# Kernel optimization log

Measured on AMD Instinct MI355X. Metric: run time of the kernel, lower is better.

The kernel has to match this reference:

```python
import jax, jax.numpy as jnp
import numpy as np

# ---- configuration matching init_kwargs ----
CTX_C = 96        # context_v_features
M_FREQS = 8       # m_encode_num_freqs
OUT_C = 45        # out_features
NDIM = 3
SIGMA = 5.0       # sigma_encode_scale
EPS = 1e-7        # TARGET_COORD_EPSILON
CX = CY = CZ = 32
QX = QY = QZ = 48
B = 1
CTX_VOX = 2.0
Q_VOX = 1.25
N_COORD = 4 * NDIM + NDIM * 2 * M_FREQS   # 60
INTERNAL = CTX_C + N_COORD                # 156


def _lin_init(k, fi, fo):
    s = 1.0 / np.sqrt(fi)
    kw, kb = jax.random.split(k)
    return (jax.random.uniform(kw, (fi, fo), jnp.float32, -s, s),
            jax.random.uniform(kb, (fo,), jnp.float32, -s, s))


def setup_inputs() -> dict:
    key = jax.random.key(0)
    ks = jax.random.split(key, 12)
    context_v = jax.random.normal(ks[0], (B, CTX_C, CX, CY, CZ), jnp.float32)
    ax = jnp.arange(CX, dtype=jnp.float32) * CTX_VOX
    gx, gy, gz = jnp.meshgrid(ax, ax, ax, indexing='ij')
    context_spatial_extent = jnp.broadcast_to(
        jnp.stack([gx, gy, gz], 0)[None], (B, 3, CX, CY, CZ)).astype(jnp.float32)
    # queries in the interior so nearest-idx + 1 stays in bounds
    query_coord = jax.random.uniform(ks[1], (B, 3, QX, QY, QZ), jnp.float32,
                                     CTX_VOX, (CX - 2) * CTX_VOX)
    query_vox_size = jnp.full((B, 3), Q_VOX, jnp.float32)
    inp = dict(context_v=context_v, context_spatial_extent=context_spatial_extent,
               query_vox_size=query_vox_size, query_coord=query_coord)
    ki = 2
    for b in range(2):
        inp[f'blk{b}_w0'], inp[f'blk{b}_b0'] = _lin_init(ks[ki], INTERNAL, CTX_C); ki += 1
        inp[f'blk{b}_w1'], inp[f'blk{b}_b1'] = _lin_init(ks[ki], CTX_C, CTX_C); ki += 1
        inp[f'blk{b}_w2'], inp[f'blk{b}_b2'] = _lin_init(ks[ki], CTX_C, CTX_C); ki += 1
    inp['post_w'], inp['post_b'] = _lin_init(ks[ki], CTX_C, OUT_C)
    return inp


def _flat(t):
    # 'b c x y z -> (b x y z) c'
    return jnp.moveaxis(t, 1, -1).reshape(-1, t.shape[1])


def _unflat(t, b, x, y, z):
    # '(b x y z) c -> b c x y z'
    return jnp.moveaxis(t.reshape(b, x, y, z, -1), -1, 1)


def _fourier(c):
    # c: (N, 3) normalized coords; geometric frequency ladder scaled by sigma
    freqs = SIGMA ** (jnp.arange(M_FREQS, dtype=c.dtype) / M_FREQS)   # (m,)
    ang = (2.0 * jnp.pi) * c[:, :, None] * freqs                      # (N,3,m)
    return jnp.concatenate([jnp.sin(ang), jnp.cos(ang)], axis=-1).reshape(c.shape[0], -1)


def _skip_block(x, coord, w0, b0, w1, b1, w2, b2):
    # SkipMLPBlock: concat(context, coord) -> 3 dense SiLU layers -> residual add
    h = jnp.concatenate([x, coord], axis=-1)
    h = jax.nn.silu(h @ w0 + b0)
    h = jax.nn.silu(h @ w1 + b1)
    h = jax.nn.silu(h @ w2 + b2)
    return x + h, coord


def _sub_grid_forward(ctx_val, ctx_coord, q_coord, ctx_vox, q_vox, p):
    # ctx_val: (B,C,X,Y,Z); coords: (B,3,X,Y,Z); ctx_vox/q_vox: (B,3,1,1,1)
    b, _, x, y, z = q_coord.shape
    rel = jnp.maximum(ctx_coord - q_coord, -ctx_vox / 2 + EPS)
    rel_norm = (rel - jnp.min(rel, axis=(2, 3, 4), keepdims=True)) / (1.5 * ctx_vox)
    enc = _fourier(_flat(rel_norm))                                   # (N, 6m)
    qv = jnp.broadcast_to(q_vox, rel_norm.shape)
    coord_feats = jnp.concatenate(
        [_flat(qv), _flat(ctx_coord), _flat(q_coord), _flat(rel_norm), enc], axis=-1)
    h = _flat(ctx_val)
    xc = coord_feats
    for i in range(2):
        h, xc = _skip_block(h, xc, p[f'blk{i}_w0'], p[f'blk{i}_b0'],
                            p[f'blk{i}_w1'], p[f'blk{i}_b1'],
                            p[f'blk{i}_w2'], p[f'blk{i}_b2'])
    pred = h @ p['post_w'] + p['post_b']
    return _unflat(pred, b, x, y, z), rel


def reference(context_v, context_spatial_extent, query_vox_size, query_coord,
              blk0_w0, blk0_b0, blk0_w1, blk0_b1, blk0_w2, blk0_b2,
              blk1_w0, blk1_b0, blk1_w1, blk1_b1, blk1_w2, blk1_b2,
              post_w, post_b):
    p = dict(blk0_w0=blk0_w0, blk0_b0=blk0_b0, blk0_w1=blk0_w1, blk0_b1=blk0_b1,
             blk0_w2=blk0_w2, blk0_b2=blk0_b2, blk1_w0=blk1_w0, blk1_b0=blk1_b0,
             blk1_w1=blk1_w1, blk1_b1=blk1_b1, blk1_w2=blk1_w2, blk1_b2=blk1_b2,
             post_w=post_w, post_b=post_b)
    bsz, _, qx, qy, qz = query_coord.shape
    cx, cy, cz = context_spatial_extent.shape[2:]
    ctx_vox = jnp.abs(context_spatial_extent[..., 1, 1, 1]
                      - context_spatial_extent[..., 0, 0, 0])[:, :, None, None, None]
    q_vox = query_vox_size[:, :, None, None, None]
    # nearest context voxel index per query point (regular grid)
    origin = context_spatial_extent[:, :, 0, 0, 0][:, :, None, None, None]
    nearest = jnp.round((query_coord - origin) / ctx_vox).astype(jnp.int32)
    xi = jnp.clip(nearest[:, 0], 0, cx - 2).reshape(-1)
    yi = jnp.clip(nearest[:, 1], 0, cy - 2).reshape(-1)
    zi = jnp.clip(nearest[:, 2], 0, cz - 2).reshape(-1)
    b_idx = jnp.broadcast_to(jnp.arange(bsz)[:, None, None, None],
                             (bsz, qx, qy, qz)).reshape(-1)
    preds = []
    rel000 = None
    for i in (0, 1):
        for j in (0, 1):
            for k in (0, 1):
                cval = context_v[b_idx, :, xi + i, yi + j, zi + k]            # (N,C) gather
                cval = _unflat(cval, bsz, qx, qy, qz)
                ccoord = context_spatial_extent[b_idx, :, xi + i, yi + j, zi + k]
                ccoord = _unflat(ccoord, bsz, qx, qy, qz)
                pred, rel = _sub_grid_forward(cval, ccoord, query_coord,
                                              ctx_vox, q_vox, p)
                preds.append(pred)
                if i == 0 and j == 0 and k == 0:
                    rel000 = rel
    preds = jnp.stack(preds, 0)   # (8, B, OUT, X, Y, Z)
    # trilinear combine over the 2x2x2 sub-window (grid_sample align_corners=True;
    # grid coord channel 0 indexes z_sub (W), 1 -> y_sub (H), 2 -> x_sub (D))
    g = jnp.clip((rel000 - 0.5) * 2.0, -1.0 + EPS, 1.0 - EPS)
    t = (g + 1.0) / 2.0
    tz, ty, tx = t[:, 0], t[:, 1], t[:, 2]
    out = jnp.zeros_like(preds[0])
    for i in (0, 1):
        wi = tx if i == 1 else 1.0 - tx
        for j in (0, 1):
            wj = ty if j == 1 else 1.0 - ty
            for k in (0, 1):
                wk = tz if k == 1 else 1.0 - tz
                out = out + preds[i * 4 + j * 2 + k] * (wi * wj * wk)[:, None]
    return out
```

## Files before the change

kernel.cpp:

```cpp
#include <hip/hip_runtime.h>
#include <hip/hip_bf16.h>

typedef unsigned short ushort_t;
typedef short short8 __attribute__((ext_vector_type(8)));
typedef short shrt4 __attribute__((ext_vector_type(4)));
typedef unsigned short ush4 __attribute__((ext_vector_type(4)));
typedef unsigned int uintx2 __attribute__((ext_vector_type(2)));
typedef float floatx4 __attribute__((ext_vector_type(4)));

#define SA 168
#define SW 104
#define NQ 110592
#define CVOL 32768

#define L0A   0
#define L0B   15360
#define A1_00 30720
#define A1_01 39936
#define A1_10 49152
#define A1_11 58368
#define PST   67584
#define WTOT  72192
#define BTOT  9216

#define WSW_OFF  64
#define BIAS_OFF 147456
#define CVT_OFF  196608

#define TXP_NB   256
#define PREP_NB  318
#define PRE_NB   (TXP_NB + PREP_NB + 432)

#if defined(__HIP_DEVICE_COMPILE__)
#define MFMA16(A, B, C) __builtin_amdgcn_mfma_f32_16x16x16bf16_1k(A, B, C, 0, 0, 0)
#else
#define MFMA16(A, B, C) (C)
#endif

#if defined(__HIP_DEVICE_COMPILE__) && __has_builtin(__builtin_amdgcn_sinf) && __has_builtin(__builtin_amdgcn_cosf) && __has_builtin(__builtin_amdgcn_fractf)
#define FAST_SINCOS 1
#else
#define FAST_SINCOS 0
#endif

__device__ __forceinline__ float bf2f(ushort_t u) { return __uint_as_float(((unsigned)u) << 16); }
__device__ __forceinline__ ushort_t f2bf(float f) {
    unsigned u = __float_as_uint(f);
    unsigned r = (u + 0x7fffu + ((u >> 16) & 1u)) >> 16;
    return (ushort_t)r;
}
__device__ __forceinline__ unsigned pkpair(float a, float b) {
#if defined(__HIP_DEVICE_COMPILE__) && __has_builtin(__builtin_amdgcn_cvt_pk_bf16_f32)
    return __builtin_bit_cast(unsigned, __builtin_amdgcn_cvt_pk_bf16_f32(a, b));
#else
    unsigned ua = __float_as_uint(a) + 0x8000u;
    unsigned ub = __float_as_uint(b) + 0x8000u;
    return __builtin_amdgcn_perm(ub, ua, 0x07060302);
#endif
}
__device__ __forceinline__ shrt4 pk4(floatx4 v) {
    uintx2 u;
    u[0] = pkpair(v[0], v[1]);
    u[1] = pkpair(v[2], v[3]);
    return __builtin_bit_cast(shrt4, u);
}
__device__ __forceinline__ unsigned encodeMin(float x) {
    unsigned u = __float_as_uint(x);
    return (u & 0x80000000u) ? ~u : (u | 0x80000000u);
}
__device__ __forceinline__ float decodeMin(unsigned key) {
    unsigned u = (key & 0x80000000u) ? (key ^ 0x80000000u) : ~key;
    return __uint_as_float(u);
}

__device__ __constant__ float FREQ[8] = {
    1.0f, 1.2228445f, 1.4953488f, 1.8285791f,
    2.2360680f, 2.7343640f, 3.3437015f, 4.0888269f
};

__global__ void decoder_pre(const float* __restrict__ cv, ushort_t* __restrict__ cvT,
                            const float* __restrict__ w00, const float* __restrict__ b00,
                            const float* __restrict__ w01, const float* __restrict__ b01,
                            const float* __restrict__ w02, const float* __restrict__ b02,
                            const float* __restrict__ w10, const float* __restrict__ b10,
                            const float* __restrict__ w11, const float* __restrict__ b11,
                            const float* __restrict__ w12, const float* __restrict__ b12,
                            const float* __restrict__ pw, ushort_t* __restrict__ wsW,
                            float* __restrict__ biasF,
                            const float* __restrict__ qc, const float* __restrict__ ext,
                            unsigned* __restrict__ keys) {
    __shared__ ushort_t ld[128 * SW];
    __shared__ unsigned mk[3];
    const int bx = blockIdx.x;
    const int tid = threadIdx.x;

    if (bx < TXP_NB) {
        int base = bx * 128;
        int cl = tid & 127, h = tid >> 7;
        #pragma unroll 4
        for (int ch = h * 48; ch < h * 48 + 48; ++ch)
            ld[cl * SW + ch] = f2bf(cv[ch * CVOL + base + cl]);
        __syncthreads();
        #pragma unroll
        for (int it = 0; it < 6; ++it) {
            int idx = it * 256 + tid;
            int r = idx / 12, c = idx - r * 12;
            *(uint4*)&cvT[(base + r) * 96 + c * 8] = *(const uint4*)&ld[r * SW + c * 8];
        }
        return;
    }
    if (bx < TXP_NB + PREP_NB) {
        int idx = (bx - TXP_NB) * 256 + tid;
        if (idx >= WTOT + BTOT) return;
        if (idx >= WTOT) {
            int t = idx - WTOT;
            int layer = t / 1536, rem = t - layer * 1536;
            int mt = rem >> 8, l2i = rem & 255;
            int lane = l2i >> 2, r = l2i & 3;
            int m = mt * 16 + (lane >> 4) * 4 + r;
            const float* B = layer == 0 ? b00 : layer == 1 ? b01 : layer == 2 ? b02
                           : layer == 3 ? b10 : layer == 4 ? b11 : b12;
            biasF[t] = B[m];
            return;
        }
        ushort_t v = 0;
        if (idx < A1_00) {
            const float* W = (idx < L0B) ? w00 : w10;
            int li = idx - ((idx < L0B) ? L0A : L0B);
            int j = li & 7, lane = (li >> 3) & 63, chunk = li >> 9;
            int kc = chunk % 5, mt = chunk / 5;
            int k = kc * 32 + (lane >> 4) * 8 + j;
            int m = mt * 16 + (lane & 15);
            if (k < 156) v = f2bf(W[k * 96 + m]);
        } else if (idx < PST) {
            const float* W = idx < A1_01 ? w01 : idx < A1_10 ? w02 : idx < A1_11 ? w11 : w12;
            int off = idx < A1_01 ? A1_00 : idx < A1_10 ? A1_01 : idx < A1_11 ? A1_10 : A1_11;
            int li = idx - off;
            int i = li & 3, kl = (li >> 2) & 1, lane = (li >> 3) & 63, chunk = li >> 9;
            int kp = chunk % 3, mt = chunk / 3;
            int k = (kp * 2 + kl) * 16 + (lane >> 4) * 4 + i;
            int m = mt * 16 + (lane & 15);
            v = f2bf(W[k * 96 + m]);
        } else {
            int li = idx - PST;
            int j = li & 7, lane = (li >> 3) & 63, chunk = li >> 9;
            int kc = chunk % 3, t = chunk / 3;
            int k = kc * 32 + (lane >> 4) * 8 + j;
            int n = t * 16 + (lane & 15);
            if (n < 45) v = f2bf(pw[k * 45 + n]);
        }
        wsW[idx] = v;
        return;
    }
    {
        int lane = tid & 63;
        if (tid < 3) mk[tid] = 0xFFFFFFFFu;
        __syncthreads();
        int p = (bx - TXP_NB - PREP_NB) * 256 + tid;
        #pragma unroll
        for (int c = 0; c < 3; ++c) {
            float org = ext[c * CVOL];
            float vox = fabsf(ext[c * CVOL + 1057] - org);
            float q = qc[c * NQ + p];
            float nf = rintf((q - org) / vox);
            int ci = (int)nf; ci = ci < 0 ? 0 : (ci > 30 ? 30 : ci);
            float base = org + (float)ci * vox - q;
            for (int off = 32; off > 0; off >>= 1) base = fminf(base, __shfl_xor(base, off));
            if (lane == 0) atomicMin(&mk[c], encodeMin(base));
        }
        __syncthreads();
        if (tid < 3) atomicMin(&keys[tid], mk[tid]);
    }
}

__global__ __launch_bounds__(256, 3) void decoder_main(
    const ushort_t* __restrict__ cvT, const float* __restrict__ ext,
    const float* __restrict__ qvx, const float* __restrict__ qc,
    const float* __restrict__ pb, const ushort_t* __restrict__ wsW,
    const float* __restrict__ biasF,
    const unsigned* __restrict__ minKeys, float* __restrict__ out)
{
    __shared__ ushort_t Xin[128 * SA];
    __shared__ ushort_t Hhat[16 * SW];
    __shared__ float ptQ[3][16], ptBase[3][16], ptT[3][16];
    __shared__ int ptCI[3][16];
    __shared__ float wcorn[16][8];

    const int tid = threadIdx.x;
    const int lane = tid & 63;
    const int wv = tid >> 6;
    const int quad = lane >> 4;
    const int l16 = lane & 15;
    const int lane8 = lane << 3, quad8 = quad * 8, quad4 = quad * 4;
    const int p0 = blockIdx.x * 16;
    const int col0 = wv * 32;

    float vox[3], org[3], lim[3], inv3v[3], qv[3], mrel[3][2];
    #pragma unroll
    for (int c = 0; c < 3; ++c) {
        org[c] = ext[c * CVOL];
        vox[c] = fabsf(ext[c * CVOL + 1057] - org[c]);
        lim[c] = -0.5f * vox[c] + 1e-7f;
        inv3v[c] = 1.0f / (1.5f * vox[c]);
        qv[c] = qvx[c];
        float mb = decodeMin(minKeys[c]);
        mrel[c][0] = fmaxf(mb, lim[c]);
        mrel[c][1] = fmaxf(mb + vox[c], lim[c]);
    }

    if (tid < 64) {
        int p = tid >> 2, c = tid & 3;
        if (c < 3) {
            float q = qc[c * NQ + p0 + p];
            float nf = rintf((q - org[c]) / vox[c]);
            int ci = (int)nf; ci = ci < 0 ? 0 : (ci > 30 ? 30 : ci);
            float base = org[c] + (float)ci * vox[c] - q;
            float rel0 = fmaxf(base, lim[c]);
            float g = fminf(fmaxf((rel0 - 0.5f) * 2.0f, -1.0f + 1e-7f), 1.0f - 1e-7f);
            ptQ[c][p] = q; ptCI[c][p] = ci; ptBase[c][p] = base; ptT[c][p] = (g + 1.0f) * 0.5f;
        }
    }
    __syncthreads();

    if (tid < 128) {
        int p = tid >> 3, corner = tid & 7;
        int i = corner >> 2, j = (corner >> 1) & 1, k = corner & 1;
        float wx = i ? ptT[2][p] : 1.0f - ptT[2][p];
        float wy = j ? ptT[1][p] : 1.0f - ptT[1][p];
        float wz = k ? ptT[0][p] : 1.0f - ptT[0][p];
        wcorn[p][corner] = wx * wy * wz;
    }

    {
        const int r = tid >> 1, h = tid & 1;
        const int p = r >> 3, corner = r & 7;
        const int i0 = corner >> 2, i1 = (corner >> 1) & 1, i2 = corner & 1;
        int io[3] = {i0, i1, i2};

        int cell = (ptCI[0][p] + i0) * 1024 + (ptCI[1][p] + i1) * 32 + ptCI[2][p] + i2;
        const uint4* src = (const uint4*)&cvT[cell * 96];
        uint4* dstX = (uint4*)&Xin[r * SA];
        #pragma unroll
        for (int cc = h * 6; cc < h * 6 + 6; ++cc) dstX[cc] = src[cc];

        float rn[3];
        #pragma unroll
        for (int c = 0; c < 3; ++c) {
            float rel = fmaxf(ptBase[c][p] + (float)io[c] * vox[c], lim[c]);
            rn[c] = (rel - mrel[c][io[c]]) * inv3v[c];
        }
        ushort_t* row = &Xin[r * SA];
        if (h == 0) {
            #pragma unroll
            for (int c = 0; c < 3; ++c) {
                row[96 + c]  = f2bf(qv[c]);
                row[99 + c]  = f2bf(org[c] + (float)(ptCI[c][p] + io[c]) * vox[c]);
                row[102 + c] = f2bf(ptQ[c][p]);
                row[105 + c] = f2bf(rn[c]);
            }
            #pragma unroll
            for (int z = 156; z < SA; ++z) row[z] = 0;
            #pragma unroll
            for (int m = 0; m < 8; ++m) {
                float ang = rn[0] * FREQ[m];
#if FAST_SINCOS
                float fr = __builtin_amdgcn_fractf(ang);
                row[108 + m] = f2bf(__builtin_amdgcn_sinf(fr));
                row[116 + m] = f2bf(__builtin_amdgcn_cosf(fr));
#else
                float s, co; sincospif(2.0f * ang, &s, &co);
                row[108 + m] = f2bf(s); row[116 + m] = f2bf(co);
#endif
            }
        } else {
            #pragma unroll
            for (int c = 1; c < 3; ++c) {
                #pragma unroll
                for (int m = 0; m < 8; ++m) {
                    float ang = rn[c] * FREQ[m];
#if FAST_SINCOS
                    float fr = __builtin_amdgcn_fractf(ang);
                    row[108 + c * 16 + m] = f2bf(__builtin_amdgcn_sinf(fr));
                    row[108 + c * 16 + 8 + m] = f2bf(__builtin_amdgcn_cosf(fr));
#else
                    float s, co; sincospif(2.0f * ang, &s, &co);
                    row[108 + c * 16 + m] = f2bf(s);
                    row[108 + c * 16 + 8 + m] = f2bf(co);
#endif
                }
            }
        }
    }
    __syncthreads();

    const int A32off[2] = {L0A, L0B};
    const int A16off[2][2] = {{A1_00, A1_01}, {A1_10, A1_11}};
    floatx4 acc[6][2];
    shrt4 bfr[6][2];

    #pragma unroll
    for (int blk = 0; blk < 2; ++blk) {
        {
            short8 bX[2][5];
            #pragma unroll
            for (int nt = 0; nt < 2; ++nt)
                #pragma unroll
                for (int kc = 0; kc < 5; ++kc)
                    bX[nt][kc] = *(const short8*)&Xin[(col0 + nt * 16 + l16) * SA + kc * 32 + quad8];
            const int lay = blk * 3;
            #pragma unroll
            for (int mt = 0; mt < 6; ++mt) {
                short8 aw[5];
                #pragma unroll
                for (int kc = 0; kc < 5; ++kc)
                    aw[kc] = *(const short8*)&wsW[A32off[blk] + ((mt * 5 + kc) << 9) + lane8];
                floatx4 bv = *(const floatx4*)&biasF[((lay * 6 + mt) << 8) + (lane << 2)];
                #pragma unroll
                for (int nt = 0; nt < 2; ++nt) {
                    floatx4 a = __builtin_amdgcn_mfma_f32_16x16x32_bf16(aw[0], bX[nt][0], bv, 0, 0, 0);
                    #pragma unroll
                    for (int kc = 1; kc < 5; ++kc)
                        a = __builtin_amdgcn_mfma_f32_16x16x32_bf16(aw[kc], bX[nt][kc], a, 0, 0, 0);
                    acc[mt][nt] = a;
                }
            }
        }
        {
            #pragma unroll
            for (int mt = 0; mt < 6; ++mt)
                #pragma unroll
                for (int nt = 0; nt < 2; ++nt) {
                    floatx4 s;
                    #pragma unroll
                    for (int r = 0; r < 4; ++r) {
                        float z = acc[mt][nt][r];
                        s[r] = z * __builtin_amdgcn_rcpf(1.0f + __expf(-z));
                    }
                    bfr[mt][nt] = pk4(s);
                }
        }
        #pragma unroll
        for (int l = 1; l < 3; ++l) {
            const int lay = blk * 3 + l;
            #pragma unroll
            for (int mt = 0; mt < 6; ++mt) {
                short8 awp[3];
                #pragma unroll
                for (int kp = 0; kp < 3; ++kp)
                    awp[kp] = *(const short8*)&wsW[A16off[blk][l - 1] + ((mt * 3 + kp) << 9) + lane8];
                floatx4 bv = *(const floatx4*)&biasF[((lay * 6 + mt) << 8) + (lane << 2)];
                #pragma unroll
                for (int nt = 0; nt < 2; ++nt) {
                    shrt4 a0 = __builtin_shufflevector(awp[0], awp[0], 0, 1, 2, 3);
                    floatx4 a = MFMA16(a0, bfr[0][nt], bv);
                    #pragma unroll
                    for (int kc = 1; kc < 6; ++kc) {
                        shrt4 af = (kc & 1)
                            ? __builtin_shufflevector(awp[kc >> 1], awp[kc >> 1], 4, 5, 6, 7)
                            : __builtin_shufflevector(awp[kc >> 1], awp[kc >> 1], 0, 1, 2, 3);
                        a = MFMA16(af, bfr[kc][nt], a);
                    }
                    acc[mt][nt] = a;
                }
            }
            if (l == 1) {
                #pragma unroll
                for (int mt = 0; mt < 6; ++mt)
                    #pragma unroll
                    for (int nt = 0; nt < 2; ++nt) {
                        floatx4 s;
                        #pragma unroll
                        for (int r = 0; r < 4; ++r) {
                            float z = acc[mt][nt][r];
                            s[r] = z * __builtin_amdgcn_rcpf(1.0f + __expf(-z));
                        }
                        bfr[mt][nt] = pk4(s);
                    }
            } else {
                #pragma unroll
                for (int mt = 0; mt < 6; ++mt)
                    #pragma unroll
                    for (int nt = 0; nt < 2; ++nt) {
                        int ca = (col0 + nt * 16 + l16) * SA + mt * 16 + quad4;
                        ush4 hu = *(const ush4*)&Xin[ca];
                        floatx4 s;
                        #pragma unroll
                        for (int r = 0; r < 4; ++r) {
                            float z = acc[mt][nt][r];
                            s[r] = z * __builtin_amdgcn_rcpf(1.0f + __expf(-z)) + bf2f(hu[r]);
                        }
                        uintx2 w;
                        w[0] = pkpair(s[0], s[1]);
                        w[1] = pkpair(s[2], s[3]);
                        *(uintx2*)&Xin[ca] = w;
                    }
            }
        }
    }

    {
        int p = tid >> 4, s6 = (tid & 15) * 6;
        float w8[8];
        #pragma unroll
        for (int c = 0; c < 8; ++c) w8[c] = wcorn[p][c];
        float sum[6] = {0.f, 0.f, 0.f, 0.f, 0.f, 0.f};
        #pragma unroll
        for (int c = 0; c < 8; ++c) {
            const unsigned* rp = (const unsigned*)&Xin[(p * 8 + c) * SA + s6];
            float w = w8[c];
            #pragma unroll
            for (int d = 0; d < 3; ++d) {
                unsigned u = rp[d];
                sum[d * 2]     += w * __uint_as_float(u << 16);
                sum[d * 2 + 1] += w * __uint_as_float(u & 0xFFFF0000u);
            }
        }
        unsigned* hp = (unsigned*)&Hhat[p * SW + s6];
        #pragma unroll
        for (int d = 0; d < 3; ++d) hp[d] = pkpair(sum[d * 2], sum[d * 2 + 1]);
    }
    __syncthreads();

    if (wv < 3) {
        const ushort_t* wb = wsW + PST;
        floatx4 pacc = {0.f, 0.f, 0.f, 0.f};
        #pragma unroll
        for (int kc = 0; kc < 3; ++kc) {
            short8 a = *(const short8*)&Hhat[l16 * SW + kc * 32 + quad8];
            short8 bfrag = *(const short8*)&wb[((wv * 3 + kc) << 9) + lane8];
            pacc = __builtin_amdgcn_mfma_f32_16x16x32_bf16(a, bfrag, pacc, 0, 0, 0);
        }
        int n = 16 * wv + l16;
        if (n < 45) {
            float bv = pb[n];
            float4 v;
            v.x = pacc[0] + bv; v.y = pacc[1] + bv; v.z = pacc[2] + bv; v.w = pacc[3] + bv;
            *(float4*)&out[n * NQ + p0 + quad * 4] = v;
        }
    }
}

extern "C" void kernel_launch(void* const* d_in, const int* in_sizes, int n_in,
                              void* d_out, int out_size, void* d_ws, size_t ws_size,
                              hipStream_t stream) {
    (void)in_sizes; (void)n_in; (void)out_size; (void)ws_size;
    const float* cv  = (const float*)d_in[0];
    const float* ext = (const float*)d_in[1];
    const float* qvx = (const float*)d_in[2];
    const float* qc  = (const float*)d_in[3];
    const float* w00 = (const float*)d_in[4];
    const float* b00 = (const float*)d_in[5];
    const float* w01 = (const float*)d_in[6];
    const float* b01 = (const float*)d_in[7];
    const float* w02 = (const float*)d_in[8];
    const float* b02 = (const float*)d_in[9];
    const float* w10 = (const float*)d_in[10];
    const float* b10 = (const float*)d_in[11];
    const float* w11 = (const float*)d_in[12];
    const float* b11 = (const float*)d_in[13];
    const float* w12 = (const float*)d_in[14];
    const float* b12 = (const float*)d_in[15];
    const float* pw  = (const float*)d_in[16];
    const float* pb  = (const float*)d_in[17];

    unsigned* keys = (unsigned*)d_ws;
    ushort_t* wsW  = (ushort_t*)((char*)d_ws + WSW_OFF);
    float* biasF   = (float*)((char*)d_ws + BIAS_OFF);
    ushort_t* cvT  = (ushort_t*)((char*)d_ws + CVT_OFF);

    hipMemsetAsync(keys, 0xFF, 12, stream);
    decoder_pre<<<PRE_NB, 256, 0, stream>>>(cv, cvT,
                                            w00, b00, w01, b01, w02, b02,
                                            w10, b10, w11, b11, w12, b12,
                                            pw, wsW, biasF, qc, ext, keys);
    decoder_main<<<6912, 256, 0, stream>>>(cvT, ext, qvx, qc,
                                           pb, wsW, biasF, keys, (float*)d_out);
}
```

Baseline: 322.9 us.

## Fold per-block-constant layer-0 features into per-corner bias and shrink input stride

The query voxel size and the context-corner coordinate features are constant per corner or linear in existing columns. They are folded algebraically into a precomputed per-corner bias for layer 0 and into merged weight rows. This shrinks the layer-0 input row from 168 to 152 columns and removes the writes of those features in the main kernel. The separate Hhat buffer is aliased into unused Xin space, and launch bounds are raised to 4 blocks per CU for occupancy. Preprocessing now splits into two kernels because the bias depends on the min-keys reduction, which adds one extra launch.

```diff
diff --git a/kernel.cpp b/kernel.cpp
--- a/kernel.cpp
+++ b/kernel.cpp
@@ -8,8 +8,7 @@
 typedef unsigned int uintx2 __attribute__((ext_vector_type(2)));
 typedef float floatx4 __attribute__((ext_vector_type(4)));
 
-#define SA 168
-#define SW 104
+#define SA 152
 #define NQ 110592
 #define CVOL 32768
 
@@ -22,14 +21,11 @@
 #define PST   67584
 #define WTOT  72192
 #define BTOT  9216
+#define B0C   1536
 
 #define WSW_OFF  64
 #define BIAS_OFF 147456
 #define CVT_OFF  196608
-
-#define TXP_NB   256
-#define PREP_NB  318
-#define PRE_NB   (TXP_NB + PREP_NB + 432)
 
 #if defined(__HIP_DEVICE_COMPILE__)
 #define MFMA16(A, B, C) __builtin_amdgcn_mfma_f32_16x16x16bf16_1k(A, B, C, 0, 0, 0)
@@ -72,91 +68,43 @@
     unsigned u = (key & 0x80000000u) ? (key ^ 0x80000000u) : ~key;
     return __uint_as_float(u);
 }
+__device__ __forceinline__ int hhAddr(int p, int c) {
+    int hi = (c >= 48) ? 1 : 0;
+    return (p * 8 + hi) * SA + 96 + c - 48 * hi;
+}
 
 __device__ __constant__ float FREQ[8] = {
     1.0f, 1.2228445f, 1.4953488f, 1.8285791f,
     2.2360680f, 2.7343640f, 3.3437015f, 4.0888269f
 };
 
-__global__ void decoder_pre(const float* __restrict__ cv, ushort_t* __restrict__ cvT,
-                            const float* __restrict__ w00, const float* __restrict__ b00,
-                            const float* __restrict__ w01, const float* __restrict__ b01,
-                            const float* __restrict__ w02, const float* __restrict__ b02,
-                            const float* __restrict__ w10, const float* __restrict__ b10,
-                            const float* __restrict__ w11, const float* __restrict__ b11,
-                            const float* __restrict__ w12, const float* __restrict__ b12,
-                            const float* __restrict__ pw, ushort_t* __restrict__ wsW,
-                            float* __restrict__ biasF,
-                            const float* __restrict__ qc, const float* __restrict__ ext,
-                            unsigned* __restrict__ keys) {
-    __shared__ ushort_t ld[128 * SW];
+__global__ void decoder_pre1(const float* __restrict__ cv, ushort_t* __restrict__ cvT,
+                             const float* __restrict__ qc, const float* __restrict__ ext,
+                             unsigned* __restrict__ keys) {
+    __shared__ ushort_t ld[128 * 104];
     __shared__ unsigned mk[3];
     const int bx = blockIdx.x;
     const int tid = threadIdx.x;
-
-    if (bx < TXP_NB) {
+    if (bx < 256) {
         int base = bx * 128;
         int cl = tid & 127, h = tid >> 7;
         #pragma unroll 4
         for (int ch = h * 48; ch < h * 48 + 48; ++ch)
-            ld[cl * SW + ch] = f2bf(cv[ch * CVOL + base + cl]);
+            ld[cl * 104 + ch] = f2bf(cv[ch * CVOL + base + cl]);
         __syncthreads();
         #pragma unroll
         for (int it = 0; it < 6; ++it) {
             int idx = it * 256 + tid;
             int r = idx / 12, c = idx - r * 12;
-            *(uint4*)&cvT[(base + r) * 96 + c * 8] = *(const uint4*)&ld[r * SW + c * 8];
-        }
-        return;
-    }
-    if (bx < TXP_NB + PREP_NB) {
-        int idx = (bx - TXP_NB) * 256 + tid;
-        if (idx >= WTOT + BTOT) return;
-        if (idx >= WTOT) {
-            int t = idx - WTOT;
-            int layer = t / 1536, rem = t - layer * 1536;
-            int mt = rem >> 8, l2i = rem & 255;
-            int lane = l2i >> 2, r = l2i & 3;
-            int m = mt * 16 + (lane >> 4) * 4 + r;
-            const float* B = layer == 0 ? b00 : layer == 1 ? b01 : layer == 2 ? b02
-                           : layer == 3 ? b10 : layer == 4 ? b11 : b12;
-            biasF[t] = B[m];
-            return;
-        }
-        ushort_t v = 0;
-        if (idx < A1_00) {
-            const float* W = (idx < L0B) ? w00 : w10;
-            int li = idx - ((idx < L0B) ? L0A : L0B);
-            int j = li & 7, lane = (li >> 3) & 63, chunk = li >> 9;
-            int kc = chunk % 5, mt = chunk / 5;
-            int k = kc * 32 + (lane >> 4) * 8 + j;
-            int m = mt * 16 + (lane & 15);
-            if (k < 156) v = f2bf(W[k * 96 + m]);
-        } else if (idx < PST) {
-            const float* W = idx < A1_01 ? w01 : idx < A1_10 ? w02 : idx < A1_11 ? w11 : w12;
-            int off = idx < A1_01 ? A1_00 : idx < A1_10 ? A1_01 : idx < A1_11 ? A1_10 : A1_11;
-            int li = idx - off;
-            int i = li & 3, kl = (li >> 2) & 1, lane = (li >> 3) & 63, chunk = li >> 9;
-            int kp = chunk % 3, mt = chunk / 3;
-            int k = (kp * 2 + kl) * 16 + (lane >> 4) * 4 + i;
-            int m = mt * 16 + (lane & 15);
-            v = f2bf(W[k * 96 + m]);
-        } else {
-            int li = idx - PST;
-            int j = li & 7, lane = (li >> 3) & 63, chunk = li >> 9;
-            int kc = chunk % 3, t = chunk / 3;
-            int k = kc * 32 + (lane >> 4) * 8 + j;
-            int n = t * 16 + (lane & 15);
-            if (n < 45) v = f2bf(pw[k * 45 + n]);
-        }
-        wsW[idx] = v;
+            *(uint4*)&cvT[(base + r) * 96 + c * 8] = *(const uint4*)&ld[r * 104 + c * 8];
+        }
         return;
     }
     {
         int lane = tid & 63;
         if (tid < 3) mk[tid] = 0xFFFFFFFFu;
         __syncthreads();
-        int p = (bx - TXP_NB - PREP_NB) * 256 + tid;
+        int p = (bx - 256) * 256 + tid;
         #pragma unroll
         for (int c = 0; c < 3; ++c) {
             float org = ext[c * CVOL];
@@ -173,15 +121,93 @@
     }
 }
 
-__global__ __launch_bounds__(256, 3) void decoder_main(
+__global__ void decoder_pre2(const float* __restrict__ w00, const float* __restrict__ b00,
+                             const float* __restrict__ w01, const float* __restrict__ b01,
+                             const float* __restrict__ w02, const float* __restrict__ b02,
+                             const float* __restrict__ w10, const float* __restrict__ b10,
+                             const float* __restrict__ w11, const float* __restrict__ b11,
+                             const float* __restrict__ w12, const float* __restrict__ b12,
+                             const float* __restrict__ pw, const float* __restrict__ qvx,
+                             const float* __restrict__ ext, const unsigned* __restrict__ keys,
+                             ushort_t* __restrict__ wsW, float* __restrict__ biasF) {
+    int idx = blockIdx.x * 256 + threadIdx.x;
+    if (idx >= WTOT + BTOT + B0C) return;
+    if (idx >= WTOT + BTOT) {
+        int t = idx - WTOT - BTOT;
+        int r = t & 3, cor = (t >> 2) & 7, quad = (t >> 5) & 3;
+        int bm = t >> 7, blk = bm / 6, mt = bm - blk * 6;
+        int ch = mt * 16 + quad * 4 + r;
+        const float* W = blk ? w10 : w00;
+        const float* B = blk ? b10 : b00;
+        float val = B[ch];
+        #pragma unroll
+        for (int c = 0; c < 3; ++c) {
+            float org = ext[c * CVOL];
+            float vox = fabsf(ext[c * CVOL + 1057] - org);
+            float lim = -0.5f * vox + 1e-7f;
+            int io = (cor >> (2 - c)) & 1;
+            float mrel = fmaxf(decodeMin(keys[c]) + (float)io * vox, lim);
+            val += W[(96 + c) * 96 + ch] * qvx[c];
+            val += W[(99 + c) * 96 + ch] * mrel;
+        }
+        biasF[BTOT + t] = val;
+        return;
+    }
+    if (idx >= WTOT) {
+        int t = idx - WTOT;
+        int layer = t / 1536, rem = t - layer * 1536;
+        int mt = rem >> 8, l2i = rem & 255;
+        int lane = l2i >> 2, r = l2i & 3;
+        int m = mt * 16 + (lane >> 4) * 4 + r;
+        const float* B = layer == 0 ? b00 : layer == 1 ? b01 : layer == 2 ? b02
+                       : layer == 3 ? b10 : layer == 4 ? b11 : b12;
+        biasF[t] = B[m];
+        return;
+    }
+    ushort_t v = 0;
+    if (idx < A1_00) {
+        const float* W = (idx < L0B) ? w00 : w10;
+        int li = idx - ((idx < L0B) ? L0A : L0B);
+        int j = li & 7, lane = (li >> 3) & 63, chunk = li >> 9;
+        int kc = chunk % 5, mt = chunk / 5;
+        int k = kc * 32 + (lane >> 4) * 8 + j;
+        int m = mt * 16 + (lane & 15);
+        float val = 0.f;
+        if (k < 96)        val = W[k * 96 + m];
+        else if (k < 99)   { int c = k - 96; val = W[(102 + c) * 96 + m] + W[(99 + c) * 96 + m]; }
+        else if (k < 102)  { int c = k - 99;
+                             float vox = fabsf(ext[c * CVOL + 1057] - ext[c * CVOL]);
+                             val = W[(105 + c) * 96 + m] + 1.5f * vox * W[(99 + c) * 96 + m]; }
+        else if (k < 150)  val = W[(k + 6) * 96 + m];
+        v = f2bf(val);
+    } else if (idx < PST) {
+        const float* W = idx < A1_01 ? w01 : idx < A1_10 ? w02 : idx < A1_11 ? w11 : w12;
+        int off = idx < A1_01 ? A1_00 : idx < A1_10 ? A1_01 : idx < A1_11 ? A1_10 : A1_11;
+        int li = idx - off;
+        int i = li & 3, kl = (li >> 2) & 1, lane = (li >> 3) & 63, chunk = li >> 9;
+        int kp = chunk % 3, mt = chunk / 3;
+        int k = (kp * 2 + kl) * 16 + (lane >> 4) * 4 + i;
+        int m = mt * 16 + (lane & 15);
+        v = f2bf(W[k * 96 + m]);
+    } else {
+        int li = idx - PST;
+        int j = li & 7, lane = (li >> 3) & 63, chunk = li >> 9;
+        int kc = chunk % 3, t = chunk / 3;
+        int k = kc * 32 + (lane >> 4) * 8 + j;
+        int n = t * 16 + (lane & 15);
+        if (n < 45) v = f2bf(pw[k * 45 + n]);
+    }
+    wsW[idx] = v;
+}
+
+__global__ __launch_bounds__(256, 4) void decoder_main(
     const ushort_t* __restrict__ cvT, const float* __restrict__ ext,
-    const float* __restrict__ qvx, const float* __restrict__ qc,
+    const float* __restrict__ qc,
     const float* __restrict__ pb, const ushort_t* __restrict__ wsW,
     const float* __restrict__ biasF,
     const unsigned* __restrict__ minKeys, float* __restrict__ out)
 {
-    __shared__ ushort_t Xin[128 * SA];
-    __shared__ ushort_t Hhat[16 * SW];
+    __shared__ ushort_t Xin[128 * SA + 16];
     __shared__ float ptQ[3][16], ptBase[3][16], ptT[3][16];
     __shared__ int ptCI[3][16];
     __shared__ float wcorn[16][8];
@@ -195,14 +221,13 @@
     const int p0 = blockIdx.x * 16;
     const int col0 = wv * 32;
 
-    float vox[3], org[3], lim[3], inv3v[3], qv[3], mrel[3][2];
+    float vox[3], org[3], lim[3], inv3v[3], mrel[3][2];
     #pragma unroll
     for (int c = 0; c < 3; ++c) {
         org[c] = ext[c * CVOL];
         vox[c] = fabsf(ext[c * CVOL + 1057] - org[c]);
         lim[c] = -0.5f * vox[c] + 1e-7f;
         inv3v[c] = 1.0f / (1.5f * vox[c]);
-        qv[c] = qvx[c];
         float mb = decodeMin(minKeys[c]);
         mrel[c][0] = fmaxf(mb, lim[c]);
         mrel[c][1] = fmaxf(mb + vox[c], lim[c]);
@@ -220,6 +245,7 @@
             ptQ[c][p] = q; ptCI[c][p] = ci; ptBase[c][p] = base; ptT[c][p] = (g + 1.0f) * 0.5f;
         }
     }
+    if (tid < 2) *(uint4*)&Xin[128 * SA + tid * 8] = (uint4){0, 0, 0, 0};
     __syncthreads();
 
     if (tid < 128) {
@@ -253,23 +279,20 @@
         if (h == 0) {
             #pragma unroll
             for (int c = 0; c < 3; ++c) {
-                row[96 + c]  = f2bf(qv[c]);
-                row[99 + c]  = f2bf(org[c] + (float)(ptCI[c][p] + io[c]) * vox[c]);
-                row[102 + c] = f2bf(ptQ[c][p]);
-                row[105 + c] = f2bf(rn[c]);
-            }
-            #pragma unroll
-            for (int z = 156; z < SA; ++z) row[z] = 0;
+                row[96 + c] = f2bf(ptQ[c][p]);
+                row[99 + c] = f2bf(rn[c]);
+            }
+            row[150] = 0; row[151] = 0;
             #pragma unroll
             for (int m = 0; m < 8; ++m) {
                 float ang = rn[0] * FREQ[m];
 #if FAST_SINCOS
                 float fr = __builtin_amdgcn_fractf(ang);
-                row[108 + m] = f2bf(__builtin_amdgcn_sinf(fr));
-                row[116 + m] = f2bf(__builtin_amdgcn_cosf(fr));
+                row[102 + m] = f2bf(__builtin_amdgcn_sinf(fr));
+                row[110 + m] = f2bf(__builtin_amdgcn_cosf(fr));
 #else
                 float s, co; sincospif(2.0f * ang, &s, &co);
-                row[108 + m] = f2bf(s); row[116 + m] = f2bf(co);
+                row[102 + m] = f2bf(s); row[110 + m] = f2bf(co);
 #endif
             }
         } else {
@@ -280,12 +303,12 @@
                     float ang = rn[c] * FREQ[m];
 #if FAST_SINCOS
                     float fr = __builtin_amdgcn_fractf(ang);
-                    row[108 + c * 16 + m] = f2bf(__builtin_amdgcn_sinf(fr));
-                    row[108 + c * 16 + 8 + m] = f2bf(__builtin_amdgcn_cosf(fr));
+                    row[102 + c * 16 + m] = f2bf(__builtin_amdgcn_sinf(fr));
+                    row[102 + c * 16 + 8 + m] = f2bf(__builtin_amdgcn_cosf(fr));
 #else
                     float s, co; sincospif(2.0f * ang, &s, &co);
-                    row[108 + c * 16 + m] = f2bf(s);
-                    row[108 + c * 16 + 8 + m] = f2bf(co);
+                    row[102 + c * 16 + m] = f2bf(s);
+                    row[102 + c * 16 + 8 + m] = f2bf(co);
 #endif
                 }
             }
@@ -295,6 +318,7 @@
 
     const int A32off[2] = {L0A, L0B};
     const int A16off[2][2] = {{A1_00, A1_01}, {A1_10, A1_11}};
+    const float* b0cT = biasF + BTOT + quad * 32 + (l16 & 7) * 4;
     floatx4 acc[6][2];
     shrt4 bfr[6][2];
 
@@ -307,14 +331,13 @@
                 #pragma unroll
                 for (int kc = 0; kc < 5; ++kc)
                     bX[nt][kc] = *(const short8*)&Xin[(col0 + nt * 16 + l16) * SA + kc * 32 + quad8];
-            const int lay = blk * 3;
             #pragma unroll
             for (int mt = 0; mt < 6; ++mt) {
                 short8 aw[5];
                 #pragma unroll
                 for (int kc = 0; kc < 5; ++kc)
                     aw[kc] = *(const short8*)&wsW[A32off[blk] + ((mt * 5 + kc) << 9) + lane8];
-                floatx4 bv = *(const floatx4*)&biasF[((lay * 6 + mt) << 8) + (lane << 2)];
+                floatx4 bv = *(const floatx4*)&b0cT[(blk * 6 + mt) << 7];
                 #pragma unroll
                 for (int nt = 0; nt < 2; ++nt) {
                     floatx4 a = __builtin_amdgcn_mfma_f32_16x16x32_bf16(aw[0], bX[nt][0], bv, 0, 0, 0);
@@ -415,9 +438,9 @@
                 sum[d * 2 + 1] += w * __uint_as_float(u & 0xFFFF0000u);
             }
         }
-        unsigned* hp = (unsigned*)&Hhat[p * SW + s6];
-        #pragma unroll
-        for (int d = 0; d < 3; ++d) hp[d] = pkpair(sum[d * 2], sum[d * 2 + 1]);
+        #pragma unroll
+        for (int d = 0; d < 3; ++d)
+            *(unsigned*)&Xin[hhAddr(p, s6 + 2 * d)] = pkpair(sum[d * 2], sum[d * 2 + 1]);
     }
     __syncthreads();
 
@@ -426,7 +449,7 @@
         floatx4 pacc = {0.f, 0.f, 0.f, 0.f};
         #pragma unroll
         for (int kc = 0; kc < 3; ++kc) {
-            short8 a = *(const short8*)&Hhat[l16 * SW + kc * 32 + quad8];
+            short8 a = *(const short8*)&Xin[hhAddr(l16, kc * 32 + quad8)];
             short8 bfrag = *(const short8*)&wb[((wv * 3 + kc) << 9) + lane8];
             pacc = __builtin_amdgcn_mfma_f32_16x16x32_bf16(a, bfrag, pacc, 0, 0, 0);
         }
@@ -469,10 +492,10 @@
     ushort_t* cvT  = (ushort_t*)((char*)d_ws + CVT_OFF);
 
     hipMemsetAsync(keys, 0xFF, 12, stream);
-    decoder_pre<<<PRE_NB, 256, 0, stream>>>(cv, cvT,
-                                            w00, b00, w01, b01, w02, b02,
-                                            w10, b10, w11, b11, w12, b12,
-                                            pw, wsW, biasF, qc, ext, keys);
-    decoder_main<<<6912, 256, 0, stream>>>(cvT, ext, qvx, qc,
+    decoder_pre1<<<688, 256, 0, stream>>>(cv, cvT, qc, ext, keys);
+    decoder_pre2<<<324, 256, 0, stream>>>(w00, b00, w01, b01, w02, b02,
+                                          w10, b10, w11, b11, w12, b12,
+                                          pw, qvx, ext, keys, wsW, biasF);
+    decoder_main<<<6912, 256, 0, stream>>>(cvT, ext, qc,
                                            pb, wsW, biasF, keys, (float*)d_out);
 }
```

Result: slower. 335.6 us (+3.9%).
